# Kernel tuning notes

Measured on AMD Instinct MI355X. Metric: run time of the kernel, lower is better.

The kernel has to match this reference:

```python
import jax, jax.numpy as jnp
import numpy as np

B, T, J, D = 64, 2048, 128, 256

def setup_inputs() -> dict:
    key = jax.random.key(0)
    k1, k2, k3 = jax.random.split(key, 3)
    H = jax.random.normal(k1, (B, T, D), dtype=jnp.float32)
    U = jax.random.normal(k2, (B, J, D), dtype=jnp.float32)
    w = jax.random.normal(k3, (3 * D, 1), dtype=jnp.float32) * 0.05
    return {"H": H, "U": U, "w": w}


def reference(H, U, w):
    # Original: tile H to (B,T,J,D), tile U to (B,T,J,D), concat [H,U,H*U] -> (B,T,J,3D),
    # then dot with w (3D,1) and squeeze -> (B,T,J).
    # Equivalent trilinear form without materializing the tiled tensor:
    # S[b,t,j] = H[b,t]@w1 + U[b,j]@w2 + (H[b,t]*w3)@U[b,j]
    d = H.shape[-1]
    wv = w[:, 0]
    w1, w2, w3 = wv[:d], wv[d:2 * d], wv[2 * d:]
    s_h = jnp.einsum('btd,d->bt', H, w1)          # (B,T)
    s_u = jnp.einsum('bjd,d->bj', U, w2)          # (B,J)
    s_hu = jnp.einsum('btd,bjd->btj', H * w3, U)  # (B,T,J)
    return s_h[:, :, None] + s_u[:, None, :] + s_hu
```

## Files before the change

### kernel.cpp

```cpp
#include <hip/hip_runtime.h>
#include <stdint.h>

#define Bb 64
#define Tt 2048
#define Jj 128
#define Dd 256


typedef __attribute__((ext_vector_type(8))) __bf16 bf16x8;
typedef __attribute__((ext_vector_type(8))) unsigned short ushort8v;
typedef __attribute__((ext_vector_type(4))) float f32x4;

__device__ __forceinline__ unsigned short f2bf(float f) {
    unsigned int u = __builtin_bit_cast(unsigned int, f);
    u += 0x7FFFu + ((u >> 16) & 1u);
    return (unsigned short)(u >> 16);
}

__device__ __forceinline__ bf16x8 pack8(const float4& a0, const float4& a1) {
    bf16x8 r;
    r[0] = (__bf16)a0.x; r[1] = (__bf16)a0.y; r[2] = (__bf16)a0.z; r[3] = (__bf16)a0.w;
    r[4] = (__bf16)a1.x; r[5] = (__bf16)a1.y; r[6] = (__bf16)a1.z; r[7] = (__bf16)a1.w;
    return r;
}

__global__ __launch_bounds__(512, 4)
void sim_fused(const float* __restrict__ H, const float* __restrict__ U,
               const float* __restrict__ w, float* __restrict__ out) {
    __shared__ ushort8v lUp[4608];
    __shared__ float lsu[Jj];

    const int tid   = threadIdx.x;
    const int wid   = tid >> 6;
    const int lane  = tid & 63;
    const int row16 = lane & 15;
    const int quad  = lane >> 4;

    const int b  = blockIdx.x >> 4;
    const int m0 = (blockIdx.x & 15) * 128 + wid * 16;

    const float* Hp = H + ((size_t)(b * Tt + m0 + row16)) * Dd + quad * 8;
    float4 hb0[3], hb1[3];
#pragma unroll
    for (int p = 0; p < 3; ++p) {
        hb0[p] = *(const float4*)(Hp + p * 32);
        hb1[p] = *(const float4*)(Hp + p * 32 + 4);
    }

    const float* Ubase = U + (size_t)b * Jj * Dd;
    const int k0 = wid * 32 + quad * 8;
#pragma unroll
    for (int p = 0; p < 9; ++p) {
        ushort8v s;
        if (p < 8) {
            const int row = p * 16 + row16;
            const float* up = Ubase + (size_t)row * Dd + k0;
            const float* wp = w + 2 * Dd + k0;
            const float4 u0 = *(const float4*)(up);
            const float4 u1 = *(const float4*)(up + 4);
            const float4 w0 = *(const float4*)(wp);
            const float4 w1 = *(const float4*)(wp + 4);
            s[0] = f2bf(u0.x * w0.x); s[1] = f2bf(u0.y * w0.y);
            s[2] = f2bf(u0.z * w0.z); s[3] = f2bf(u0.w * w0.w);
            s[4] = f2bf(u1.x * w1.x); s[5] = f2bf(u1.y * w1.y);
            s[6] = f2bf(u1.z * w1.z); s[7] = f2bf(u1.w * w1.w);
        } else {
            const bool n0 = row16 == 0;
#pragma unroll
            for (int e = 0; e < 8; ++e)
                s[e] = n0 ? f2bf(w[k0 + e]) : (unsigned short)0;
        }
        lUp[(p * 8 + wid) * 64 + lane] = s;
    }

    {
        const int row = tid >> 2;
        const int c0  = (tid & 3) * 64;
        const float* up = Ubase + (size_t)row * Dd + c0;
        const float* wp = w + Dd + c0;
        float ssum = 0.f;
#pragma unroll
        for (int i = 0; i < 16; ++i) {
            const float4 u = *(const float4*)(up + i * 4);
            const float4 v = *(const float4*)(wp + i * 4);
            ssum += u.x * v.x + u.y * v.y + u.z * v.z + u.w * v.w;
        }
        ssum += __shfl_xor(ssum, 1);
        ssum += __shfl_xor(ssum, 2);
        if ((tid & 3) == 0) lsu[row] = ssum;
    }

    f32x4 acc[9];
#pragma unroll
    for (int j = 0; j < 9; ++j) acc[j] = (f32x4){0.f, 0.f, 0.f, 0.f};

    __syncthreads();

#pragma unroll
    for (int ks = 0; ks < 8; ++ks) {
        const int slot = ks % 3;
        const float4 h0 = hb0[slot];
        const float4 h1 = hb1[slot];
        if (ks < 5) {
            hb0[slot] = *(const float4*)(Hp + (ks + 3) * 32);
            hb1[slot] = *(const float4*)(Hp + (ks + 3) * 32 + 4);
        }

        const bf16x8 af = pack8(h0, h1);
#pragma unroll
        for (int j = 0; j < 9; ++j) {
            const bf16x8 bf = __builtin_bit_cast(bf16x8, lUp[(j * 8 + ks) * 64 + lane]);
            acc[j] = __builtin_amdgcn_mfma_f32_16x16x32_bf16(af, bf, acc[j], 0, 0, 0);
        }
    }

    float shv[4];
#pragma unroll
    for (int rg = 0; rg < 4; ++rg)
        shv[rg] = __shfl(acc[8][rg], quad * 16);

    float* outW = out + ((size_t)(b * Tt + m0)) * Jj;
#pragma unroll
    for (int j = 0; j < 8; ++j) {
        const int col = j * 16 + row16;
        const float suv = lsu[col];
#pragma unroll
        for (int rg = 0; rg < 4; ++rg)
            outW[(size_t)(quad * 4 + rg) * Jj + col] = acc[j][rg] + shv[rg] + suv;
    }
}

extern "C" void kernel_launch(void* const* d_in, const int* in_sizes, int n_in,
                              void* d_out, int out_size, void* d_ws, size_t ws_size,
                              hipStream_t stream) {
    const float* H = (const float*)d_in[0];
    const float* U = (const float*)d_in[1];
    const float* w = (const float*)d_in[2];
    float* out = (float*)d_out;
    (void)d_ws; (void)ws_size;

    sim_fused<<<Bb * 16, 512, 0, stream>>>(H, U, w, out);
}
```

Before: 244.0 us.

## Process two M-tiles per block and fuse U·w2 reduction into staging loads

Each block now covers 256 rows of T instead of 128 and loops over two 128-row tiles, so the U staging into LDS is amortized over twice as much work and the grid is halved. The s_u dot product is computed from the U values already loaded for the bf16 staging, which removes the second pass over U; partial sums are reduced through shuffles and an LDS array. This costs an extra barrier, more LDS, and fewer blocks, which may lower occupancy and latency hiding.

```diff
diff --git a/kernel.cpp b/kernel.cpp
--- a/kernel.cpp
+++ b/kernel.cpp
@@ -28,7 +28,8 @@
 void sim_fused(const float* __restrict__ H, const float* __restrict__ U,
                const float* __restrict__ w, float* __restrict__ out) {
     __shared__ ushort8v lUp[4608];
-    __shared__ float lsu[Jj];
+    __shared__ float    lsuP[8 * Jj];
+    __shared__ float    lsu[Jj];
 
     const int tid   = threadIdx.x;
     const int wid   = tid >> 6;
@@ -36,58 +37,63 @@
     const int row16 = lane & 15;
     const int quad  = lane >> 4;
 
-    const int b  = blockIdx.x >> 4;
-    const int m0 = (blockIdx.x & 15) * 128 + wid * 16;
+    const int b     = blockIdx.x >> 3;
+    const int mbase = (blockIdx.x & 7) * 256;
 
-    const float* Hp = H + ((size_t)(b * Tt + m0 + row16)) * Dd + quad * 8;
+    const float* Hbase = H + ((size_t)(b * Tt + mbase + wid * 16 + row16)) * Dd + quad * 8;
     float4 hb0[3], hb1[3];
 #pragma unroll
     for (int p = 0; p < 3; ++p) {
-        hb0[p] = *(const float4*)(Hp + p * 32);
-        hb1[p] = *(const float4*)(Hp + p * 32 + 4);
+        hb0[p] = *(const float4*)(Hbase + p * 32);
+        hb1[p] = *(const float4*)(Hbase + p * 32 + 4);
     }
 
+    const int k0 = wid * 32 + quad * 8;
+    const float4 w1a = *(const float4*)(w + k0);
+    const float4 w1b = *(const float4*)(w + k0 + 4);
+    const float4 w2a = *(const float4*)(w + Dd + k0);
+    const float4 w2b = *(const float4*)(w + Dd + k0 + 4);
+    const float4 w3a = *(const float4*)(w + 2 * Dd + k0);
+    const float4 w3b = *(const float4*)(w + 2 * Dd + k0 + 4);
+
     const float* Ubase = U + (size_t)b * Jj * Dd;
-    const int k0 = wid * 32 + quad * 8;
+    float sup[8];
 #pragma unroll
-    for (int p = 0; p < 9; ++p) {
+    for (int p = 0; p < 8; ++p) {
+        const float* up = Ubase + (size_t)(p * 16 + row16) * Dd + k0;
+        const float4 u0 = *(const float4*)(up);
+        const float4 u1 = *(const float4*)(up + 4);
         ushort8v s;
-        if (p < 8) {
-            const int row = p * 16 + row16;
-            const float* up = Ubase + (size_t)row * Dd + k0;
-            const float* wp = w + 2 * Dd + k0;
-            const float4 u0 = *(const float4*)(up);
-            const float4 u1 = *(const float4*)(up + 4);
-            const float4 w0 = *(const float4*)(wp);
-            const float4 w1 = *(const float4*)(wp + 4);
-            s[0] = f2bf(u0.x * w0.x); s[1] = f2bf(u0.y * w0.y);
-            s[2] = f2bf(u0.z * w0.z); s[3] = f2bf(u0.w * w0.w);
-            s[4] = f2bf(u1.x * w1.x); s[5] = f2bf(u1.y * w1.y);
-            s[6] = f2bf(u1.z * w1.z); s[7] = f2bf(u1.w * w1.w);
-        } else {
-            const bool n0 = row16 == 0;
+        s[0] = f2bf(u0.x * w3a.x); s[1] = f2bf(u0.y * w3a.y);
+        s[2] = f2bf(u0.z * w3a.z); s[3] = f2bf(u0.w * w3a.w);
+        s[4] = f2bf(u1.x * w3b.x); s[5] = f2bf(u1.y * w3b.y);
+        s[6] = f2bf(u1.z * w3b.z); s[7] = f2bf(u1.w * w3b.w);
+        lUp[(p * 8 + wid) * 64 + lane] = s;
+        sup[p] = u0.x * w2a.x + u0.y * w2a.y + u0.z * w2a.z + u0.w * w2a.w
+               + u1.x * w2b.x + u1.y * w2b.y + u1.z * w2b.z + u1.w * w2b.w;
+    }
+    {
+        const bool n0 = row16 == 0;
+        ushort8v s;
+        s[0] = n0 ? f2bf(w1a.x) : (unsigned short)0;
+        s[1] = n0 ? f2bf(w1a.y) : (unsigned short)0;
+        s[2] = n0 ? f2bf(w1a.z) : (unsigned short)0;
+        s[3] = n0 ? f2bf(w1a.w) : (unsigned short)0;
+        s[4] = n0 ? f2bf(w1b.x) : (unsigned short)0;
+        s[5] = n0 ? f2bf(w1b.y) : (unsigned short)0;
+        s[6] = n0 ? f2bf(w1b.z) : (unsigned short)0;
+        s[7] = n0 ? f2bf(w1b.w) : (unsigned short)0;
+        lUp[(8 * 8 + wid) * 64 + lane] = s;
+    }
 #pragma unroll
-            for (int e = 0; e < 8; ++e)
-                s[e] = n0 ? f2bf(w[k0 + e]) : (unsigned short)0;
-        }
-        lUp[(p * 8 + wid) * 64 + lane] = s;
+    for (int p = 0; p < 8; ++p) {
+        sup[p] += __shfl_xor(sup[p], 16);
+        sup[p] += __shfl_xor(sup[p], 32);
     }
-
-    {
-        const int row = tid >> 2;
-        const int c0  = (tid & 3) * 64;
-        const float* up = Ubase + (size_t)row * Dd + c0;
-        const float* wp = w + Dd + c0;
-        float ssum = 0.f;
+    if (quad == 0) {
 #pragma unroll
-        for (int i = 0; i < 16; ++i) {
-            const float4 u = *(const float4*)(up + i * 4);
-            const float4 v = *(const float4*)(wp + i * 4);
-            ssum += u.x * v.x + u.y * v.y + u.z * v.z + u.w * v.w;
-        }
-        ssum += __shfl_xor(ssum, 1);
-        ssum += __shfl_xor(ssum, 2);
-        if ((tid & 3) == 0) lsu[row] = ssum;
+        for (int p = 0; p < 8; ++p)
+            lsuP[wid * Jj + p * 16 + row16] = sup[p];
     }
 
     f32x4 acc[9];
@@ -96,37 +102,56 @@
 
     __syncthreads();
 
+    if (tid < Jj) {
+        float s = 0.f;
 #pragma unroll
-    for (int ks = 0; ks < 8; ++ks) {
-        const int slot = ks % 3;
-        const float4 h0 = hb0[slot];
-        const float4 h1 = hb1[slot];
-        if (ks < 5) {
-            hb0[slot] = *(const float4*)(Hp + (ks + 3) * 32);
-            hb1[slot] = *(const float4*)(Hp + (ks + 3) * 32 + 4);
+        for (int ww = 0; ww < 8; ++ww) s += lsuP[ww * Jj + tid];
+        lsu[tid] = s;
+    }
+    __syncthreads();
+
+#pragma unroll
+    for (int mt = 0; mt < 2; ++mt) {
+#pragma unroll
+        for (int ks = 0; ks < 8; ++ks) {
+            const int kk   = mt * 8 + ks;
+            const int slot = kk % 3;
+            const float4 h0 = hb0[slot];
+            const float4 h1 = hb1[slot];
+            if (kk < 13) {
+                const float* np = Hbase + (size_t)(((kk + 3) >> 3) * 128 * Dd)
+                                        + ((kk + 3) & 7) * 32;
+                hb0[slot] = *(const float4*)(np);
+                hb1[slot] = *(const float4*)(np + 4);
+            }
+
+            const bf16x8 af = pack8(h0, h1);
+#pragma unroll
+            for (int j = 0; j < 9; ++j) {
+                const bf16x8 bf = __builtin_bit_cast(bf16x8, lUp[(j * 8 + ks) * 64 + lane]);
+                acc[j] = __builtin_amdgcn_mfma_f32_16x16x32_bf16(af, bf, acc[j], 0, 0, 0);
+            }
         }
 
-        const bf16x8 af = pack8(h0, h1);
-#pragma unroll
-        for (int j = 0; j < 9; ++j) {
-            const bf16x8 bf = __builtin_bit_cast(bf16x8, lUp[(j * 8 + ks) * 64 + lane]);
-            acc[j] = __builtin_amdgcn_mfma_f32_16x16x32_bf16(af, bf, acc[j], 0, 0, 0);
-        }
-    }
-
-    float shv[4];
-#pragma unroll
-    for (int rg = 0; rg < 4; ++rg)
-        shv[rg] = __shfl(acc[8][rg], quad * 16);
-
-    float* outW = out + ((size_t)(b * Tt + m0)) * Jj;
-#pragma unroll
-    for (int j = 0; j < 8; ++j) {
-        const int col = j * 16 + row16;
-        const float suv = lsu[col];
+        float shv[4];
 #pragma unroll
         for (int rg = 0; rg < 4; ++rg)
-            outW[(size_t)(quad * 4 + rg) * Jj + col] = acc[j][rg] + shv[rg] + suv;
+            shv[rg] = __shfl(acc[8][rg], quad * 16);
+
+        float* outW = out + ((size_t)(b * Tt + mbase + mt * 128 + wid * 16)) * Jj;
+#pragma unroll
+        for (int j = 0; j < 8; ++j) {
+            const int col = j * 16 + row16;
+            const float suv = lsu[col];
+#pragma unroll
+            for (int rg = 0; rg < 4; ++rg)
+                outW[(size_t)(quad * 4 + rg) * Jj + col] = acc[j][rg] + shv[rg] + suv;
+        }
+
+        if (mt == 0) {
+#pragma unroll
+            for (int j = 0; j < 9; ++j) acc[j] = (f32x4){0.f, 0.f, 0.f, 0.f};
+        }
     }
 }
 
@@ -139,5 +164,5 @@
     float* out = (float*)d_out;
     (void)d_ws; (void)ws_size;
 
-    sim_fused<<<Bb * 16, 512, 0, stream>>>(H, U, w, out);
+    sim_fused<<<Bb * 8, 512, 0, stream>>>(H, U, w, out);
 }
```

Result: faster. 225.7 us (-7.5%).
